# Kernel optimization log

Measured on AMD Instinct MI355X. Metric: run time of the kernel, lower is better.

## Reference

```python
import jax, jax.numpy as jnp
import numpy as np

B, S, D = 4, 4096, 1024
E = 8            # num_expert_extra + num_expert_proto
F = 2 * D        # ffn_mult * dim
EPS = 1e-5


def setup_inputs() -> dict:
    key = jax.random.key(0)
    ks = jax.random.split(key, 8)
    sc = 0.02
    return {
        "inputs": jax.random.normal(ks[0], (B, S, D), jnp.float32),
        "Wr": jax.random.normal(ks[1], (D, E), jnp.float32) * sc,   # router (no bias)
        "W1": jax.random.normal(ks[2], (E, D, F), jnp.float32) * sc,
        "b1": jnp.zeros((E, F), jnp.float32),
        "gamma": jnp.ones((E, F), jnp.float32),
        "beta": jnp.zeros((E, F), jnp.float32),
        "W2": jax.random.normal(ks[3], (E, F, D), jnp.float32) * sc,
        "b2": jnp.zeros((E, D), jnp.float32),
    }


def reference(inputs, Wr, W1, b1, gamma, beta, W2, b2):
    b, s, d = inputs.shape
    top_k = max(1, int(1.0 * s / E))  # capacity_factor=1.0

    # router: [b, s, e]
    logits = jnp.einsum('bsd,de->bse', inputs, Wr)
    probs = jax.nn.softmax(logits.astype(jnp.float32), axis=-1)

    # expert-choice top-k over tokens: [b, e, k]
    weights, idx = jax.lax.top_k(probs.transpose(0, 2, 1), top_k)

    # gather dispatched tokens: [b, e, k, d]
    bix = jnp.arange(b)[:, None, None]
    xg = inputs[bix, idx]

    # per-expert FFN: fc2(LN(gelu(fc1(x)))) (subln, dropout=eval identity)
    h = jnp.einsum('bekd,edf->bekf', xg, W1) + b1[None, :, None, :]
    h = jax.nn.gelu(h, approximate=False)
    mu = jnp.mean(h, axis=-1, keepdims=True)
    var = jnp.mean(jnp.square(h - mu), axis=-1, keepdims=True)
    h = (h - mu) * jax.lax.rsqrt(var + EPS)
    h = h * gamma[None, :, None, :] + beta[None, :, None, :]
    out = jnp.einsum('bekf,efd->bekd', h, W2) + b2[None, :, None, :]

    # weighted scatter-add back to token positions
    val = weights[..., None].astype(inputs.dtype) * out
    results = jnp.zeros_like(inputs).at[bix, idx].add(val)
    return results, logits
```

## Files before the change

### kernel.cpp

```cpp
#include <hip/hip_runtime.h>
#include <hip/hip_bf16.h>

#define B_ 4
#define S_ 4096
#define D_ 1024
#define E_ 8
#define F_ 2048
#define TK_ 512

typedef unsigned short u16;
typedef unsigned int u32;
typedef u16 u16x4 __attribute__((ext_vector_type(4)));
typedef u16 u16x8 __attribute__((ext_vector_type(8)));
typedef short s16x8 __attribute__((ext_vector_type(8)));
typedef float f32x4 __attribute__((ext_vector_type(4)));

__device__ __forceinline__ u16 f2bf(float f) {
  u32 u = __builtin_bit_cast(u32, f);
  u32 r = (u + 0x7fffu + ((u >> 16) & 1u)) >> 16;
  return (u16)r;
}
__device__ __forceinline__ float b2f(u16 h) {
  return __builtin_bit_cast(float, ((u32)h) << 16);
}
__device__ __forceinline__ void gload16(const u16* g, const u16* l) {
  __builtin_amdgcn_global_load_lds((const __attribute__((address_space(1))) void*)g,
                                   (__attribute__((address_space(3))) void*)l, 16, 0, 0);
}
__device__ __forceinline__ f32x4 mfma_bf16(s16x8 a, s16x8 b, f32x4 c) {
  return __builtin_amdgcn_mfma_f32_16x16x32_bf16(a, b, c, 0, 0, 0);
}
__device__ __forceinline__ float gelu_t(float v) {
  float t = v * (1.5957691216f + 0.0713548162726f * v * v);
  return v / (1.f + __expf(-t));
}

__global__ __launch_bounds__(256) void rc_kernel(const float* __restrict__ x,
                                                 const float* __restrict__ Wr,
                                                 float* __restrict__ logits,
                                                 float* __restrict__ probs,
                                                 u16* __restrict__ xb,
                                                 float* __restrict__ results) {
  __shared__ float wr[D_ * E_];
  for (int i = threadIdx.x; i < D_ * E_; i += 256) wr[i] = Wr[i];
  __syncthreads();
  int lane = threadIdx.x & 63;
  int wid = threadIdx.x >> 6;
  int token = blockIdx.x * 4 + wid;
  const float* xr = x + (size_t)token * D_;
  u16* xo = xb + (size_t)token * D_;
  float* ro = results + (size_t)token * D_;
  float acc[E_];
#pragma unroll
  for (int e = 0; e < E_; ++e) acc[e] = 0.f;
#pragma unroll
  for (int q = 0; q < 4; ++q) {
    int d0 = q * 256 + lane * 4;
    float4 v = *(const float4*)(xr + d0);
    u16x4 st;
    st[0] = f2bf(v.x); st[1] = f2bf(v.y); st[2] = f2bf(v.z); st[3] = f2bf(v.w);
    *(u16x4*)(xo + d0) = st;
    *(float4*)(ro + d0) = make_float4(0.f, 0.f, 0.f, 0.f);
    float xv[4] = {v.x, v.y, v.z, v.w};
    const float* w0 = &wr[d0 * E_];
#pragma unroll
    for (int j = 0; j < 4; ++j) {
#pragma unroll
      for (int e = 0; e < E_; ++e) acc[e] += xv[j] * w0[j * E_ + e];
    }
  }
#pragma unroll
  for (int e = 0; e < E_; ++e) {
#pragma unroll
    for (int off = 32; off; off >>= 1) acc[e] += __shfl_down(acc[e], off);
  }
  if (lane == 0) {
    float4 o0 = make_float4(acc[0], acc[1], acc[2], acc[3]);
    float4 o1 = make_float4(acc[4], acc[5], acc[6], acc[7]);
    *(float4*)(logits + (size_t)token * E_) = o0;
    *(float4*)(logits + (size_t)token * E_ + 4) = o1;
    float mx = acc[0];
#pragma unroll
    for (int t = 1; t < 8; ++t) mx = fmaxf(mx, acc[t]);
    float sum = 0.f;
    float pe[8];
#pragma unroll
    for (int t = 0; t < 8; ++t) { pe[t] = expf(acc[t] - mx); sum += pe[t]; }
    float inv = 1.f / sum;
    float4 p0 = make_float4(pe[0] * inv, pe[1] * inv, pe[2] * inv, pe[3] * inv);
    float4 p1 = make_float4(pe[4] * inv, pe[5] * inv, pe[6] * inv, pe[7] * inv);
    *(float4*)(probs + (size_t)token * E_) = p0;
    *(float4*)(probs + (size_t)token * E_ + 4) = p1;
  }
}

__device__ __forceinline__ void suffix_scan(u32* h, int n, int tid) {
  for (int d = 1; d < n; d <<= 1) {
    u32 v[2];
    int c = 0;
    for (int i = tid; i < n; i += 1024) v[c++] = (i + d < n) ? h[i + d] : 0;
    __syncthreads();
    c = 0;
    for (int i = tid; i < n; i += 1024) h[i] += v[c++];
    __syncthreads();
  }
}

__global__ __launch_bounds__(1024) void topk_kernel(const float* __restrict__ probs,
                                                    int* __restrict__ idx,
                                                    float* __restrict__ wts) {
  int be = blockIdx.x, b = be >> 3, e = be & 7;
  __shared__ u32 keys[S_];
  __shared__ u32 hist[2048];
  __shared__ u32 tcnt[1024];
  __shared__ u32 sb, sneed, scnt;
  int tid = threadIdx.x;
  const float* pr = probs + (size_t)b * S_ * E_ + e;
  for (int s = tid; s < S_; s += 1024) keys[s] = __builtin_bit_cast(u32, pr[(size_t)s * E_]);
  if (tid == 0) scnt = 0;

  hist[tid] = 0; hist[tid + 1024] = 0;
  __syncthreads();
  for (int s = tid; s < S_; s += 1024) atomicAdd(&hist[keys[s] >> 21], 1u);
  __syncthreads();
  suffix_scan(hist, 2048, tid);
  for (int i = tid; i < 2048; i += 1024) {
    u32 nxt = (i + 1 < 2048) ? hist[i + 1] : 0;
    if (hist[i] >= (u32)TK_ && nxt < (u32)TK_) { sb = (u32)i; sneed = TK_ - nxt; }
  }
  __syncthreads();
  u32 b1 = sb, need1 = sneed;
  __syncthreads();

  hist[tid] = 0; hist[tid + 1024] = 0;
  __syncthreads();
  for (int s = tid; s < S_; s += 1024)
    if ((keys[s] >> 21) == b1) atomicAdd(&hist[(keys[s] >> 10) & 2047u], 1u);
  __syncthreads();
  suffix_scan(hist, 2048, tid);
  for (int i = tid; i < 2048; i += 1024) {
    u32 nxt = (i + 1 < 2048) ? hist[i + 1] : 0;
    if (hist[i] >= need1 && nxt < need1) { sb = (u32)i; sneed = need1 - nxt; }
  }
  __syncthreads();
  u32 p2 = (b1 << 11) | sb, need2 = sneed;
  __syncthreads();

  if (tid < 1024) hist[tid] = 0;
  __syncthreads();
  for (int s = tid; s < S_; s += 1024)
    if ((keys[s] >> 10) == p2) atomicAdd(&hist[keys[s] & 1023u], 1u);
  __syncthreads();
  suffix_scan(hist, 1024, tid);
  for (int i = tid; i < 1024; i += 1024) {
    u32 nxt = (i + 1 < 1024) ? hist[i + 1] : 0;
    if (hist[i] >= need2 && nxt < need2) { sb = (u32)i; sneed = need2 - nxt; }
  }
  __syncthreads();
  u32 T = (p2 << 10) | sb;
  u32 needT = sneed;

  for (int s = tid; s < S_; s += 1024) {
    if (keys[s] > T) {
      u32 p = atomicAdd(&scnt, 1u);
      idx[be * TK_ + p] = s;
      wts[be * TK_ + p] = __builtin_bit_cast(float, keys[s]);
    }
  }
  u32 myc = 0;
#pragma unroll
  for (int j = 0; j < 4; ++j) myc += (keys[tid * 4 + j] == T) ? 1u : 0u;
  tcnt[tid] = myc;
  __syncthreads();
  for (int d = 1; d < 1024; d <<= 1) {
    u32 v = (tid >= d) ? tcnt[tid - d] : 0;
    __syncthreads();
    tcnt[tid] += v;
    __syncthreads();
  }
  u32 rank = tcnt[tid] - myc;
#pragma unroll
  for (int j = 0; j < 4; ++j) {
    int s = tid * 4 + j;
    if (keys[s] == T) {
      if (rank < needT) {
        u32 p = atomicAdd(&scnt, 1u);
        idx[be * TK_ + p] = s;
        wts[be * TK_ + p] = __builtin_bit_cast(float, T);
      }
      rank++;
    }
  }
}

__global__ __launch_bounds__(256) void transpose_cvt_kernel(const float* __restrict__ src,
                                                            u16* __restrict__ dst,
                                                            int R, int C,
                                                            const float* __restrict__ scale,
                                                            const float* __restrict__ beta,
                                                            float* __restrict__ Bd,
                                                            float* __restrict__ G) {
  __shared__ float tile[32][33];
  int z = blockIdx.z;
  const float* s = src + (size_t)z * R * C;
  u16* d = dst + (size_t)z * R * C;
  int r0 = blockIdx.x * 32, c0 = blockIdx.y * 32;
  int xx = threadIdx.x & 31, yy = threadIdx.x >> 5;
#pragma unroll
  for (int q = 0; q < 4; ++q)
    tile[yy + q * 8][xx] = s[(size_t)(r0 + yy + q * 8) * C + c0 + xx];
  __syncthreads();
  float sc = scale ? scale[(size_t)z * R + r0 + xx] : 1.f;
#pragma unroll
  for (int q = 0; q < 4; ++q)
    d[(size_t)(c0 + yy + q * 8) * R + r0 + xx] = f2bf(sc * tile[xx][yy + q * 8]);
  if (Bd != nullptr) {
    __syncthreads();
    if (threadIdx.x < 32) {
      float smb = 0.f, smg = 0.f;
      const float* br = beta + (size_t)z * R + r0;
      const float* gr = scale + (size_t)z * R + r0;
#pragma unroll
      for (int f = 0; f < 32; ++f) {
        smb += br[f] * tile[f][threadIdx.x];
        smg += gr[f] * tile[f][threadIdx.x];
      }
      unsafeAtomicAdd(&Bd[(size_t)z * C + c0 + threadIdx.x], smb);
      unsafeAtomicAdd(&G[(size_t)z * C + c0 + threadIdx.x], smg);
    }
  }
}

__device__ __forceinline__ void kloop97(const u16* const pa[4], const u16* const pb[4],
                                        u16* As, u16* Bs, f32x4 acc[4][4], int NT,
                                        int wid, const int aoff[4], const int boff[4],
                                        int sk0, int sk1) {
  int ldst = wid * 512;
  for (int t = 0; t < NT; ++t) {
    int k0 = t * 64;
#pragma unroll
    for (int q = 0; q < 4; ++q) gload16(pa[q] + k0, As + q * 2048 + ldst);
#pragma unroll
    for (int q = 0; q < 4; ++q) gload16(pb[q] + k0, Bs + q * 2048 + ldst);
    asm volatile("s_waitcnt vmcnt(0)" ::: "memory");
    __builtin_amdgcn_s_barrier();
    s16x8 aF[4], bF[4];
#pragma unroll
    for (int kk = 0; kk < 2; ++kk) {
      int sk = kk ? sk1 : sk0;
#pragma unroll
      for (int f = 0; f < 4; ++f) aF[f] = *(const s16x8*)&As[aoff[f] + sk];
#pragma unroll
      for (int g = 0; g < 4; ++g) bF[g] = *(const s16x8*)&Bs[boff[g] + sk];
      __builtin_amdgcn_s_setprio(1);
#pragma unroll
      for (int f = 0; f < 4; ++f)
#pragma unroll
        for (int g = 0; g < 4; ++g) acc[f][g] = mfma_bf16(aF[f], bF[g], acc[f][g]);
      __builtin_amdgcn_s_setprio(0);
    }
    __builtin_amdgcn_s_barrier();
  }
}

__global__ __launch_bounds__(256, 2) void gemm1_kernel(const u16* __restrict__ xb,
                                                       const u16* __restrict__ W1t,
                                                       const float* __restrict__ b1,
                                                       const int* __restrict__ idx,
                                                       u16* __restrict__ hbuf,
                                                       float2* __restrict__ stats2) {
  int p = blockIdx.x;
  int e = p & 7, slot = p >> 3;
  int tm = slot & 3, bb = (slot >> 2) & 3, tn = slot >> 4;
  int be = bb * 8 + e;
  int t0 = tm * 128, n0 = tn * 128;
  int tid = threadIdx.x, lane = tid & 63, wid = tid >> 6;
  int wm = wid >> 1, wn = wid & 1;
  int cidx = lane & 15, kq = lane >> 4;
  __shared__ u16 As[128 * 64];
  __shared__ u16 Bs[128 * 64];
  __shared__ float2 sm[128][2];

  int srow = tid >> 3;
  int kc = (tid & 7) ^ (srow & 7);
  const u16* pa[4];
  const u16* pb[4];
  const u16* bsrc = W1t + (size_t)e * F_ * D_;
#pragma unroll
  for (int q = 0; q < 4; ++q) {
    int tok = idx[be * TK_ + t0 + q * 32 + srow];
    pa[q] = xb + ((size_t)bb * S_ + tok) * D_ + kc * 8;
    pb[q] = bsrc + (size_t)(n0 + q * 32 + srow) * D_ + kc * 8;
  }
  int aoff[4], boff[4];
#pragma unroll
  for (int f = 0; f < 4; ++f) {
    aoff[f] = (wm * 64 + f * 16 + cidx) * 64;
    boff[f] = (wn * 64 + f * 16 + cidx) * 64;
  }
  int sk0 = (kq ^ (cidx & 7)) * 8;
  int sk1 = ((4 + kq) ^ (cidx & 7)) * 8;

  f32x4 acc[4][4];
#pragma unroll
  for (int f = 0; f < 4; ++f)
#pragma unroll
    for (int g = 0; g < 4; ++g) acc[f][g] = (f32x4){0.f, 0.f, 0.f, 0.f};

  kloop97(pa, pb, As, Bs, acc, D_ / 64, wid, aoff, boff, sk0, sk1);

  float bias[4];
#pragma unroll
  for (int g = 0; g < 4; ++g) bias[g] = b1[e * F_ + n0 + wn * 64 + g * 16 + cidx];
  size_t hbase = (size_t)be * TK_ * F_;
#pragma unroll
  for (int f = 0; f < 4; ++f) {
#pragma unroll
    for (int r = 0; r < 4; ++r) {
      int lr = wm * 64 + f * 16 + kq * 4 + r;
      size_t hb = hbase + (size_t)(t0 + lr) * F_ + n0 + wn * 64 + cidx;
      float vs = 0.f, vss = 0.f;
#pragma unroll
      for (int g = 0; g < 4; ++g) {
        float v = acc[f][g][r] + bias[g];
        float gl = gelu_t(v);
        hbuf[hb + g * 16] = f2bf(gl);
        vs += gl;
        vss += gl * gl;
      }
#pragma unroll
      for (int off = 1; off < 16; off <<= 1) {
        vs += __shfl_xor(vs, off);
        vss += __shfl_xor(vss, off);
      }
      if (cidx == 0) {
        float2 o; o.x = vs; o.y = vss;
        sm[lr][wn] = o;
      }
    }
  }
  __syncthreads();
  if (tid < 128) {
    float2 a = sm[tid][0], b = sm[tid][1];
    float2 o; o.x = a.x + b.x; o.y = a.y + b.y;
    stats2[((size_t)be * TK_ + t0 + tid) * 16 + tn] = o;
  }
}

__global__ __launch_bounds__(256, 2) void gemm2_kernel(const u16* __restrict__ hbuf,
                                                       const u16* __restrict__ W2g,
                                                       const float* __restrict__ b2,
                                                       const int* __restrict__ idx,
                                                       const float* __restrict__ wts,
                                                       float* __restrict__ results,
                                                       const float2* __restrict__ stats2,
                                                       const float* __restrict__ G,
                                                       const float* __restrict__ Bd) {
  int p = blockIdx.x;
  int e = p & 7, slot = p >> 3;
  int tn = slot & 7, tm = (slot >> 3) & 3, bb = slot >> 5;
  int be = bb * 8 + e;
  int t0 = tm * 128, n0 = tn * 128;
  int tid = threadIdx.x, lane = tid & 63, wid = tid >> 6;
  int wm = wid >> 1, wn = wid & 1;
  int cidx = lane & 15, kq = lane >> 4;
  __shared__ u16 As[128 * 64];
  __shared__ u16 Bs[128 * 64];
  __shared__ float smean[128];
  __shared__ float srstd[128];

  if (tid < 128) {
    const float2* sp = stats2 + ((size_t)be * TK_ + t0 + tid) * 16;
    float sum = 0.f, ss = 0.f;
#pragma unroll
    for (int j = 0; j < 16; ++j) {
      float2 v = sp[j];
      sum += v.x;
      ss += v.y;
    }
    float mean = sum * (1.f / F_);
    float var = ss * (1.f / F_) - mean * mean;
    smean[tid] = mean;
    srstd[tid] = rsqrtf(var + 1e-5f);
  }
  __syncthreads();

  int srow = tid >> 3;
  int kc = (tid & 7) ^ (srow & 7);
  const u16* pa[4];
  const u16* pb[4];
  const u16* asrc = hbuf + (size_t)be * TK_ * F_;
  const u16* bsrc = W2g + (size_t)e * D_ * F_;
#pragma unroll
  for (int q = 0; q < 4; ++q) {
    pa[q] = asrc + (size_t)(t0 + q * 32 + srow) * F_ + kc * 8;
    pb[q] = bsrc + (size_t)(n0 + q * 32 + srow) * F_ + kc * 8;
  }
  int aoff[4], boff[4];
#pragma unroll
  for (int f = 0; f < 4; ++f) {
    aoff[f] = (wm * 64 + f * 16 + cidx) * 64;
    boff[f] = (wn * 64 + f * 16 + cidx) * 64;
  }
  int sk0 = (kq ^ (cidx & 7)) * 8;
  int sk1 = ((4 + kq) ^ (cidx & 7)) * 8;

  f32x4 acc[4][4];
#pragma unroll
  for (int f = 0; f < 4; ++f)
#pragma unroll
    for (int g = 0; g < 4; ++g) acc[f][g] = (f32x4){0.f, 0.f, 0.f, 0.f};

  kloop97(pa, pb, As, Bs, acc, F_ / 64, wid, aoff, boff, sk0, sk1);

  int cb = n0 + wn * 64 + cidx;
  float b2v[4], Gv[4], Bdv[4];
#pragma unroll
  for (int g = 0; g < 4; ++g) {
    b2v[g] = b2[e * D_ + cb + g * 16];
    Gv[g] = G[e * D_ + cb + g * 16];
    Bdv[g] = Bd[e * D_ + cb + g * 16];
  }
#pragma unroll
  for (int f = 0; f < 4; ++f) {
#pragma unroll
    for (int r = 0; r < 4; ++r) {
      int lr = wm * 64 + f * 16 + kq * 4 + r;
      int trow = t0 + lr;
      int tok = idx[be * TK_ + trow];
      float wv = wts[be * TK_ + trow];
      float mean = smean[lr], rstd = srstd[lr];
      float* rrow = results + ((size_t)bb * S_ + tok) * D_ + cb;
#pragma unroll
      for (int g = 0; g < 4; ++g) {
        float out = rstd * acc[f][g][r] - rstd * mean * Gv[g] + Bdv[g] + b2v[g];
        unsafeAtomicAdd(rrow + g * 16, wv * out);
      }
    }
  }
}

extern "C" void kernel_launch(void* const* d_in, const int* in_sizes, int n_in,
                              void* d_out, int out_size, void* d_ws, size_t ws_size,
                              hipStream_t stream) {
  const float* x = (const float*)d_in[0];
  const float* Wr = (const float*)d_in[1];
  const float* W1 = (const float*)d_in[2];
  const float* b1 = (const float*)d_in[3];
  const float* gamma = (const float*)d_in[4];
  const float* beta = (const float*)d_in[5];
  const float* W2 = (const float*)d_in[6];
  const float* b2 = (const float*)d_in[7];

  float* results = (float*)d_out;
  float* logits = results + (size_t)B_ * S_ * D_;

  char* ws = (char*)d_ws;
  const size_t OFF_IDX = 0;
  const size_t OFF_WTS = OFF_IDX + (size_t)B_ * E_ * TK_ * 4;
  const size_t OFF_ST = OFF_WTS + (size_t)B_ * E_ * TK_ * 4;
  const size_t OFF_G = OFF_ST + (size_t)B_ * E_ * TK_ * 16 * 8;
  const size_t OFF_BD = OFF_G + (size_t)E_ * D_ * 4;
  const size_t OFF_P = OFF_BD + (size_t)E_ * D_ * 4;
  const size_t OFF_R0 = OFF_P + (size_t)B_ * S_ * E_ * 4;
  const size_t OFF_R1 = OFF_R0 + (size_t)E_ * D_ * F_ * 2;
  const size_t OFF_H = OFF_R1 + (size_t)E_ * D_ * F_ * 2;
  const size_t NEED = OFF_H + (size_t)B_ * E_ * TK_ * F_ * 2;
  if (ws_size < NEED) return;

  int* idx = (int*)(ws + OFF_IDX);
  float* wts = (float*)(ws + OFF_WTS);
  float2* stats2 = (float2*)(ws + OFF_ST);
  float* G = (float*)(ws + OFF_G);
  float* Bd = (float*)(ws + OFF_BD);
  float* probs = (float*)(ws + OFF_P);
  u16* xb = (u16*)(ws + OFF_R0);
  u16* W2g = (u16*)(ws + OFF_R0);
  u16* W1t = (u16*)(ws + OFF_R1);
  u16* hbuf = (u16*)(ws + OFF_H);

  rc_kernel<<<dim3(B_ * S_ / 4), 256, 0, stream>>>(x, Wr, logits, probs, xb, results);
  topk_kernel<<<dim3(B_ * E_), 1024, 0, stream>>>(probs, idx, wts);
  transpose_cvt_kernel<<<dim3(D_ / 32, F_ / 32, E_), 256, 0, stream>>>(
      W1, W1t, D_, F_, nullptr, nullptr, nullptr, nullptr);
  gemm1_kernel<<<dim3(2048), 256, 0, stream>>>(xb, W1t, b1, idx, hbuf, stats2);
  hipMemsetAsync(G, 0, (size_t)2 * E_ * D_ * 4, stream);
  transpose_cvt_kernel<<<dim3(F_ / 32, D_ / 32, E_), 256, 0, stream>>>(
      W2, W2g, F_, D_, gamma, beta, Bd, G);
  gemm2_kernel<<<dim3(1024), 256, 0, stream>>>(hbuf, W2g, b2, idx, wts, results,
                                               stats2, G, Bd);
}
```

Baseline: 315.5 us.

## Split GEMM2 reduction dimension in two and fold G/Bd zeroing into router kernel

GEMM2 now splits its F reduction into two halves, doubling the grid to 2048 blocks. Each half atomically adds its partial product into the results, and only the first half adds the bias and mean-correction terms. This raises parallelism and occupancy for a GEMM that had only 1024 blocks, at the cost of twice as many float atomics on the output. The separate memset of G/Bd is removed and the zeroing is done by the first 16 blocks of the router kernel, saving one launch.

```diff
diff --git a/kernel.cpp b/kernel.cpp
--- a/kernel.cpp
+++ b/kernel.cpp
@@ -40,9 +40,14 @@
                                                  float* __restrict__ logits,
                                                  float* __restrict__ probs,
                                                  u16* __restrict__ xb,
-                                                 float* __restrict__ results) {
+                                                 float* __restrict__ results,
+                                                 float* __restrict__ GBd) {
   __shared__ float wr[D_ * E_];
   for (int i = threadIdx.x; i < D_ * E_; i += 256) wr[i] = Wr[i];
+  if (blockIdx.x < 16) {
+    float4 z = make_float4(0.f, 0.f, 0.f, 0.f);
+    *(float4*)(GBd + (size_t)blockIdx.x * 1024 + threadIdx.x * 4) = z;
+  }
   __syncthreads();
   int lane = threadIdx.x & 63;
   int wid = threadIdx.x >> 6;
@@ -358,7 +363,8 @@
                                                        const float* __restrict__ Bd) {
   int p = blockIdx.x;
   int e = p & 7, slot = p >> 3;
-  int tn = slot & 7, tm = (slot >> 3) & 3, bb = slot >> 5;
+  int kh2 = slot & 1;
+  int tn = (slot >> 1) & 7, tm = (slot >> 4) & 3, bb = slot >> 6;
   int be = bb * 8 + e;
   int t0 = tm * 128, n0 = tn * 128;
   int tid = threadIdx.x, lane = tid & 63, wid = tid >> 6;
@@ -387,14 +393,15 @@
 
   int srow = tid >> 3;
   int kc = (tid & 7) ^ (srow & 7);
+  int kb = kh2 * 1024;
   const u16* pa[4];
   const u16* pb[4];
   const u16* asrc = hbuf + (size_t)be * TK_ * F_;
   const u16* bsrc = W2g + (size_t)e * D_ * F_;
 #pragma unroll
   for (int q = 0; q < 4; ++q) {
-    pa[q] = asrc + (size_t)(t0 + q * 32 + srow) * F_ + kc * 8;
-    pb[q] = bsrc + (size_t)(n0 + q * 32 + srow) * F_ + kc * 8;
+    pa[q] = asrc + (size_t)(t0 + q * 32 + srow) * F_ + kb + kc * 8;
+    pb[q] = bsrc + (size_t)(n0 + q * 32 + srow) * F_ + kb + kc * 8;
   }
   int aoff[4], boff[4];
 #pragma unroll
@@ -411,15 +418,17 @@
 #pragma unroll
     for (int g = 0; g < 4; ++g) acc[f][g] = (f32x4){0.f, 0.f, 0.f, 0.f};
 
-  kloop97(pa, pb, As, Bs, acc, F_ / 64, wid, aoff, boff, sk0, sk1);
+  kloop97(pa, pb, As, Bs, acc, 1024 / 64, wid, aoff, boff, sk0, sk1);
 
   int cb = n0 + wn * 64 + cidx;
   float b2v[4], Gv[4], Bdv[4];
-#pragma unroll
-  for (int g = 0; g < 4; ++g) {
-    b2v[g] = b2[e * D_ + cb + g * 16];
-    Gv[g] = G[e * D_ + cb + g * 16];
-    Bdv[g] = Bd[e * D_ + cb + g * 16];
+  if (kh2 == 0) {
+#pragma unroll
+    for (int g = 0; g < 4; ++g) {
+      b2v[g] = b2[e * D_ + cb + g * 16];
+      Gv[g] = G[e * D_ + cb + g * 16];
+      Bdv[g] = Bd[e * D_ + cb + g * 16];
+    }
   }
 #pragma unroll
   for (int f = 0; f < 4; ++f) {
@@ -429,12 +438,21 @@
       int trow = t0 + lr;
       int tok = idx[be * TK_ + trow];
       float wv = wts[be * TK_ + trow];
-      float mean = smean[lr], rstd = srstd[lr];
+      float rstd = srstd[lr];
+      float coef = wv * rstd;
       float* rrow = results + ((size_t)bb * S_ + tok) * D_ + cb;
-#pragma unroll
-      for (int g = 0; g < 4; ++g) {
-        float out = rstd * acc[f][g][r] - rstd * mean * Gv[g] + Bdv[g] + b2v[g];
-        unsafeAtomicAdd(rrow + g * 16, wv * out);
+      if (kh2 == 0) {
+        float mean = smean[lr];
+#pragma unroll
+        for (int g = 0; g < 4; ++g) {
+          float val = coef * acc[f][g][r] + wv * (Bdv[g] + b2v[g] - rstd * mean * Gv[g]);
+          unsafeAtomicAdd(rrow + g * 16, val);
+        }
+      } else {
+#pragma unroll
+        for (int g = 0; g < 4; ++g) {
+          unsafeAtomicAdd(rrow + g * 16, coef * acc[f][g][r]);
+        }
       }
     }
   }
@@ -479,14 +497,13 @@
   u16* W1t = (u16*)(ws + OFF_R1);
   u16* hbuf = (u16*)(ws + OFF_H);
 
-  rc_kernel<<<dim3(B_ * S_ / 4), 256, 0, stream>>>(x, Wr, logits, probs, xb, results);
+  rc_kernel<<<dim3(B_ * S_ / 4), 256, 0, stream>>>(x, Wr, logits, probs, xb, results, G);
   topk_kernel<<<dim3(B_ * E_), 1024, 0, stream>>>(probs, idx, wts);
   transpose_cvt_kernel<<<dim3(D_ / 32, F_ / 32, E_), 256, 0, stream>>>(
       W1, W1t, D_, F_, nullptr, nullptr, nullptr, nullptr);
   gemm1_kernel<<<dim3(2048), 256, 0, stream>>>(xb, W1t, b1, idx, hbuf, stats2);
-  hipMemsetAsync(G, 0, (size_t)2 * E_ * D_ * 4, stream);
   transpose_cvt_kernel<<<dim3(F_ / 32, D_ / 32, E_), 256, 0, stream>>>(
       W2, W2g, F_, D_, gamma, beta, Bd, G);
-  gemm2_kernel<<<dim3(1024), 256, 0, stream>>>(hbuf, W2g, b2, idx, wts, results,
+  gemm2_kernel<<<dim3(2048), 256, 0, stream>>>(hbuf, W2g, b2, idx, wts, results,
                                                stats2, G, Bd);
 }
```

New measurement: 352.8 us. +11.8%, slower.

## Fuse weight transposes into topk and gemm1 launches, move zero-init

Applied to the files above, without the earlier changes.

The W1 transpose/convert is folded into the top-k kernel as extra blocks, and that kernel also zeroes the results buffer. The W2 transpose with gamma scaling and the Bd/G reductions runs as extra blocks of gemm1 when the workspace is large enough to hold a separate W2g buffer. Zeroing of G/Bd moves into the router kernel, replacing the memset. The aim is fewer launches and letting the weight conversion overlap the small top-k grid and the GEMM. In exchange, gemm1 carries dead shared-memory branches, and the top-k kernel runs 16384 small 1024-thread blocks with one element per thread.

```diff
diff --git a/kernel.cpp b/kernel.cpp
--- a/kernel.cpp
+++ b/kernel.cpp
@@ -40,16 +40,19 @@
                                                  float* __restrict__ logits,
                                                  float* __restrict__ probs,
                                                  u16* __restrict__ xb,
-                                                 float* __restrict__ results) {
+                                                 float* __restrict__ GBd) {
   __shared__ float wr[D_ * E_];
   for (int i = threadIdx.x; i < D_ * E_; i += 256) wr[i] = Wr[i];
+  if (blockIdx.x < 16) {
+    float4 z = make_float4(0.f, 0.f, 0.f, 0.f);
+    *(float4*)(GBd + (size_t)blockIdx.x * 1024 + threadIdx.x * 4) = z;
+  }
   __syncthreads();
   int lane = threadIdx.x & 63;
   int wid = threadIdx.x >> 6;
   int token = blockIdx.x * 4 + wid;
   const float* xr = x + (size_t)token * D_;
   u16* xo = xb + (size_t)token * D_;
-  float* ro = results + (size_t)token * D_;
   float acc[E_];
 #pragma unroll
   for (int e = 0; e < E_; ++e) acc[e] = 0.f;
@@ -60,7 +63,6 @@
     u16x4 st;
     st[0] = f2bf(v.x); st[1] = f2bf(v.y); st[2] = f2bf(v.z); st[3] = f2bf(v.w);
     *(u16x4*)(xo + d0) = st;
-    *(float4*)(ro + d0) = make_float4(0.f, 0.f, 0.f, 0.f);
     float xv[4] = {v.x, v.y, v.z, v.w};
     const float* w0 = &wr[d0 * E_];
 #pragma unroll
@@ -106,15 +108,32 @@
   }
 }
 
-__global__ __launch_bounds__(1024) void topk_kernel(const float* __restrict__ probs,
-                                                    int* __restrict__ idx,
-                                                    float* __restrict__ wts) {
-  int be = blockIdx.x, b = be >> 3, e = be & 7;
+__global__ __launch_bounds__(1024) void tk_tr_kernel(const float* __restrict__ probs,
+                                                     int* __restrict__ idx,
+                                                     float* __restrict__ wts,
+                                                     const float* __restrict__ W1,
+                                                     u16* __restrict__ W1t,
+                                                     float* __restrict__ results) {
   __shared__ u32 keys[S_];
   __shared__ u32 hist[2048];
   __shared__ u32 tcnt[1024];
   __shared__ u32 sb, sneed, scnt;
   int tid = threadIdx.x;
+  if (blockIdx.x >= 32) {
+    int t = blockIdx.x - 32;
+    int z = t >> 11, rem = t & 2047;
+    int r0 = (rem & 31) * 32, c0 = (rem >> 5) * 32;
+    float(*tile)[33] = (float(*)[33])keys;
+    const float* s = W1 + (size_t)z * D_ * F_;
+    u16* d = W1t + (size_t)z * D_ * F_;
+    int xx = tid & 31, yy = tid >> 5;
+    tile[yy][xx] = s[(size_t)(r0 + yy) * F_ + c0 + xx];
+    results[(size_t)t * 1024 + tid] = 0.f;
+    __syncthreads();
+    d[(size_t)(c0 + yy) * D_ + r0 + xx] = f2bf(tile[xx][yy]);
+    return;
+  }
+  int be = blockIdx.x, b = be >> 3, e = be & 7;
   const float* pr = probs + (size_t)b * S_ * E_ + e;
   for (int s = tid; s < S_; s += 1024) keys[s] = __builtin_bit_cast(u32, pr[(size_t)s * E_]);
   if (tid == 0) scnt = 0;
@@ -210,24 +229,22 @@
   for (int q = 0; q < 4; ++q)
     tile[yy + q * 8][xx] = s[(size_t)(r0 + yy + q * 8) * C + c0 + xx];
   __syncthreads();
-  float sc = scale ? scale[(size_t)z * R + r0 + xx] : 1.f;
+  float sc = scale[(size_t)z * R + r0 + xx];
 #pragma unroll
   for (int q = 0; q < 4; ++q)
     d[(size_t)(c0 + yy + q * 8) * R + r0 + xx] = f2bf(sc * tile[xx][yy + q * 8]);
-  if (Bd != nullptr) {
-    __syncthreads();
-    if (threadIdx.x < 32) {
-      float smb = 0.f, smg = 0.f;
-      const float* br = beta + (size_t)z * R + r0;
-      const float* gr = scale + (size_t)z * R + r0;
-#pragma unroll
-      for (int f = 0; f < 32; ++f) {
-        smb += br[f] * tile[f][threadIdx.x];
-        smg += gr[f] * tile[f][threadIdx.x];
-      }
-      unsafeAtomicAdd(&Bd[(size_t)z * C + c0 + threadIdx.x], smb);
-      unsafeAtomicAdd(&G[(size_t)z * C + c0 + threadIdx.x], smg);
-    }
+  __syncthreads();
+  if (threadIdx.x < 32) {
+    float smb = 0.f, smg = 0.f;
+    const float* br = beta + (size_t)z * R + r0;
+    const float* gr = scale + (size_t)z * R + r0;
+#pragma unroll
+    for (int f = 0; f < 32; ++f) {
+      smb += br[f] * tile[f][threadIdx.x];
+      smg += gr[f] * tile[f][threadIdx.x];
+    }
+    unsafeAtomicAdd(&Bd[(size_t)z * C + c0 + threadIdx.x], smb);
+    unsafeAtomicAdd(&G[(size_t)z * C + c0 + threadIdx.x], smg);
   }
 }
 
@@ -268,18 +285,56 @@
                                                        const float* __restrict__ b1,
                                                        const int* __restrict__ idx,
                                                        u16* __restrict__ hbuf,
-                                                       float2* __restrict__ stats2) {
+                                                       float2* __restrict__ stats2,
+                                                       const float* __restrict__ W2,
+                                                       const float* __restrict__ gamma,
+                                                       const float* __restrict__ beta,
+                                                       u16* __restrict__ W2g,
+                                                       float* __restrict__ Bd,
+                                                       float* __restrict__ G) {
+  __shared__ u16 As[128 * 64];
+  __shared__ u16 Bs[128 * 64];
+  __shared__ float2 sm[128][2];
+  int tid = threadIdx.x;
+  if (blockIdx.x >= 2048) {
+    int t = blockIdx.x - 2048;
+    int z = t >> 11, rem = t & 2047;
+    int r0 = (rem & 63) * 32, c0 = (rem >> 6) * 32;
+    float(*tile)[33] = (float(*)[33])As;
+    const float* s = W2 + (size_t)z * F_ * D_;
+    u16* dd = W2g + (size_t)z * D_ * F_;
+    int xx = tid & 31, yy = tid >> 5;
+#pragma unroll
+    for (int q = 0; q < 4; ++q)
+      tile[yy + q * 8][xx] = s[(size_t)(r0 + yy + q * 8) * D_ + c0 + xx];
+    __syncthreads();
+    float sc = gamma[(size_t)z * F_ + r0 + xx];
+#pragma unroll
+    for (int q = 0; q < 4; ++q)
+      dd[(size_t)(c0 + yy + q * 8) * F_ + r0 + xx] = f2bf(sc * tile[xx][yy + q * 8]);
+    __syncthreads();
+    if (tid < 32) {
+      float smb = 0.f, smg = 0.f;
+      const float* br = beta + (size_t)z * F_ + r0;
+      const float* gr = gamma + (size_t)z * F_ + r0;
+#pragma unroll
+      for (int f = 0; f < 32; ++f) {
+        smb += br[f] * tile[f][tid];
+        smg += gr[f] * tile[f][tid];
+      }
+      unsafeAtomicAdd(&Bd[(size_t)z * D_ + c0 + tid], smb);
+      unsafeAtomicAdd(&G[(size_t)z * D_ + c0 + tid], smg);
+    }
+    return;
+  }
   int p = blockIdx.x;
   int e = p & 7, slot = p >> 3;
   int tm = slot & 3, bb = (slot >> 2) & 3, tn = slot >> 4;
   int be = bb * 8 + e;
   int t0 = tm * 128, n0 = tn * 128;
-  int tid = threadIdx.x, lane = tid & 63, wid = tid >> 6;
+  int lane = tid & 63, wid = tid >> 6;
   int wm = wid >> 1, wn = wid & 1;
   int cidx = lane & 15, kq = lane >> 4;
-  __shared__ u16 As[128 * 64];
-  __shared__ u16 Bs[128 * 64];
-  __shared__ float2 sm[128][2];
 
   int srow = tid >> 3;
   int kc = (tid & 7) ^ (srow & 7);
@@ -466,7 +521,10 @@
   const size_t OFF_R1 = OFF_R0 + (size_t)E_ * D_ * F_ * 2;
   const size_t OFF_H = OFF_R1 + (size_t)E_ * D_ * F_ * 2;
   const size_t NEED = OFF_H + (size_t)B_ * E_ * TK_ * F_ * 2;
+  const size_t OFF_W2G = NEED;
+  const size_t NEED_BIG = OFF_W2G + (size_t)E_ * D_ * F_ * 2;
   if (ws_size < NEED) return;
+  bool bigws = ws_size >= NEED_BIG;
 
   int* idx = (int*)(ws + OFF_IDX);
   float* wts = (float*)(ws + OFF_WTS);
@@ -475,18 +533,21 @@
   float* Bd = (float*)(ws + OFF_BD);
   float* probs = (float*)(ws + OFF_P);
   u16* xb = (u16*)(ws + OFF_R0);
-  u16* W2g = (u16*)(ws + OFF_R0);
   u16* W1t = (u16*)(ws + OFF_R1);
   u16* hbuf = (u16*)(ws + OFF_H);
-
-  rc_kernel<<<dim3(B_ * S_ / 4), 256, 0, stream>>>(x, Wr, logits, probs, xb, results);
-  topk_kernel<<<dim3(B_ * E_), 1024, 0, stream>>>(probs, idx, wts);
-  transpose_cvt_kernel<<<dim3(D_ / 32, F_ / 32, E_), 256, 0, stream>>>(
-      W1, W1t, D_, F_, nullptr, nullptr, nullptr, nullptr);
-  gemm1_kernel<<<dim3(2048), 256, 0, stream>>>(xb, W1t, b1, idx, hbuf, stats2);
-  hipMemsetAsync(G, 0, (size_t)2 * E_ * D_ * 4, stream);
-  transpose_cvt_kernel<<<dim3(F_ / 32, D_ / 32, E_), 256, 0, stream>>>(
-      W2, W2g, F_, D_, gamma, beta, Bd, G);
+  u16* W2g = bigws ? (u16*)(ws + OFF_W2G) : (u16*)(ws + OFF_R0);
+
+  rc_kernel<<<dim3(B_ * S_ / 4), 256, 0, stream>>>(x, Wr, logits, probs, xb, G);
+  tk_tr_kernel<<<dim3(32 + 16384), 1024, 0, stream>>>(probs, idx, wts, W1, W1t, results);
+  if (bigws) {
+    gemm1_kernel<<<dim3(2048 + 16384), 256, 0, stream>>>(xb, W1t, b1, idx, hbuf, stats2,
+                                                         W2, gamma, beta, W2g, Bd, G);
+  } else {
+    gemm1_kernel<<<dim3(2048), 256, 0, stream>>>(xb, W1t, b1, idx, hbuf, stats2,
+                                                 W2, gamma, beta, W2g, Bd, G);
+    transpose_cvt_kernel<<<dim3(F_ / 32, D_ / 32, E_), 256, 0, stream>>>(
+        W2, W2g, F_, D_, gamma, beta, Bd, G);
+  }
   gemm2_kernel<<<dim3(1024), 256, 0, stream>>>(hbuf, W2g, b2, idx, wts, results,
                                                stats2, G, Bd);
 }
```

New measurement: 310.7 us (median of 2 runs). Within noise of the previous version (-1.5%).
